# Performance work log

Measured on AMD Instinct MI355X. Metric: run time of the kernel, lower is better.

The kernel has to match this reference:

```python
import jax, jax.numpy as jnp
import numpy as np

P = 1024   # number of partitions / local models (n_terms)
K = 9      # local neighborhood size (in_dim of each LocalDNN)
W = 10     # LocalDNN width
B = 16384  # batch
F = 1024   # input feature dim (lattice sites)


def setup_inputs() -> dict:
    key = jax.random.key(0)
    ks = jax.random.split(key, 9)
    x = jax.random.normal(ks[0], (B, F), dtype=jnp.float32)
    idx = jax.random.randint(ks[1], (P, K), 0, F)  # parameter_map: per-partition feature indices
    # stacked LocalDNN parameters (one tiny MLP per partition)
    s1 = 1.0 / np.sqrt(K)
    s2 = 1.0 / np.sqrt(W)
    W1 = jax.random.uniform(ks[2], (P, K, W), jnp.float32, -s1, s1)
    b1 = jax.random.uniform(ks[3], (P, W), jnp.float32, -s1, s1)
    W2 = jax.random.uniform(ks[4], (P, W, W), jnp.float32, -s2, s2)
    b2 = jax.random.uniform(ks[5], (P, W), jnp.float32, -s2, s2)
    W3 = jax.random.uniform(ks[6], (P, W), jnp.float32, -s2, s2)   # Linear(width,1) weight
    b3 = jax.random.uniform(ks[7], (P,), jnp.float32, -s2, s2)
    sP = 1.0 / np.sqrt(P)
    w_last = jax.random.uniform(ks[8], (P,), jnp.float32, -sP, sP)  # Linear(n_terms,1,bias=False)
    return {"x": x, "idx": idx, "W1": W1, "b1": b1, "W2": W2, "b2": b2,
            "W3": W3, "b3": b3, "w_last": w_last}


def reference(x, idx, W1, b1, W2, b2, W3, b3, w_last):
    # local_map: gather per-partition features -> [B, P, K]
    xg = x[:, idx]
    # LocalDNN (depth=2): Linear(K,W) -> tanh -> Linear(W,W) -> (dropout eval no-op) -> Linear(W,1)
    h = jnp.tanh(jnp.einsum('bpk,pkw->bpw', xg, W1) + b1)      # [B,P,W]
    h = jnp.einsum('bpw,pwv->bpv', h, W2) + b2                  # [B,P,W]
    local_out = jnp.einsum('bpw,pw->bp', h, W3) + b3            # concat of per-model outputs [B,P]
    y = local_out @ w_last                                      # last_layer, flatten -> [B]
    return jnp.stack((y, jnp.full_like(y, jnp.sum(jnp.abs(w_last)))))
```

## Files before the change

kernel.cpp:

```cpp
#include <hip/hip_runtime.h>
#include <cstdint>
#include <cstddef>

#define B_TOT   16384
#define F_DIM   1024
#define P_TOT   1024
#define K_IN    9
#define W_H     10
#define TB      128
#define THREADS 1024
#define NWAVE   16
#define PGRP    2
#define PPB     (P_TOT / PGRP)
#define LSTR    1028
#define XS_BYTES (TB * LSTR)

#define REC_DW   64
#define TANH_C   2.8853900817779268f
#define F8_MAX   448.0f

typedef float f32x2 __attribute__((ext_vector_type(2)));

__device__ __forceinline__ float fast_exp2(float x) {
#if __has_builtin(__builtin_amdgcn_exp2f)
    return __builtin_amdgcn_exp2f(x);
#else
    return exp2f(x);
#endif
}
__device__ __forceinline__ float fast_rcp(float x) {
#if __has_builtin(__builtin_amdgcn_rcpf)
    return __builtin_amdgcn_rcpf(x);
#else
    return 1.0f / x;
#endif
}
__device__ __forceinline__ float sigm_r(float z) {
    return fast_rcp(fast_exp2(z) + 1.0f);
}
__device__ __forceinline__ f32x2 pkfma(f32x2 a, f32x2 b, f32x2 c) {
#if __has_builtin(__builtin_elementwise_fma)
    return __builtin_elementwise_fma(a, b, c);
#else
    return f32x2{fmaf(a[0], b[0], c[0]), fmaf(a[1], b[1], c[1])};
#endif
}
__device__ __forceinline__ f32x2 unpk8_w0(uint32_t u) {
#if __has_builtin(__builtin_amdgcn_cvt_pk_f32_fp8)
    auto v = __builtin_amdgcn_cvt_pk_f32_fp8((int)u, false);
    return f32x2{v[0], v[1]};
#else
    return f32x2{__builtin_amdgcn_cvt_f32_fp8((int)u, 0),
                 __builtin_amdgcn_cvt_f32_fp8((int)u, 1)};
#endif
}
__device__ __forceinline__ f32x2 unpk8_w1(uint32_t u) {
#if __has_builtin(__builtin_amdgcn_cvt_pk_f32_fp8)
    auto v = __builtin_amdgcn_cvt_pk_f32_fp8((int)u, true);
    return f32x2{v[0], v[1]};
#else
    return f32x2{__builtin_amdgcn_cvt_f32_fp8((int)u, 2),
                 __builtin_amdgcn_cvt_f32_fp8((int)u, 3)};
#endif
}
__device__ __forceinline__ f32x2 unpk8s(uint32_t u, int word) {
    return word ? unpk8_w1(u) : unpk8_w0(u);
}
__device__ __forceinline__ uint32_t pk2(float a0, float a1, float b0, float b1) {
    uint32_t u = (uint32_t)__builtin_amdgcn_cvt_pk_fp8_f32(a0, a1, 0, false);
    u = (uint32_t)__builtin_amdgcn_cvt_pk_fp8_f32(b0, b1, (int)u, true);
    return u;
}

__device__ __forceinline__ uint32_t rec_dword(
    int p, int dw, const int* idx,
    const float* w1, const float* b1, const float* w2, const float* b2,
    const float* w3, const float* b3, const float* wl,
    float s1, float q1)
{
    if (dw < 9)  return (uint32_t)idx[p * 9 + dw];
    if (dw == 9) return __float_as_uint(s1 * TANH_C);
    if (dw < 20) return __float_as_uint(b1[p * 10 + (dw - 10)] * TANH_C);
    if (dw == 20) {
        float bb = b3[p];
        for (int v = 0; v < 10; ++v) bb = fmaf(b2[p * 10 + v], w3[v], bb);
        float s = 0.f;
        for (int w = 0; w < 10; ++w)
            for (int v = 0; v < 10; ++v)
                s = fmaf(w2[w * 10 + v], w3[v], s);
        return __float_as_uint(wl[p] * (s + bb));
    }
    if (dw < 31) {
        const int w = dw - 21;
        float s = 0.f;
        for (int v = 0; v < 10; ++v) s = fmaf(w2[w * 10 + v], w3[v], s);
        return __float_as_uint(-2.0f * wl[p] * s);
    }
    if (dw < 32) return 0;
    if (dw < 55) {
        const int d = dw - 32, t0 = 2 * d, t1 = t0 + 1;
        const int e0 = (t0 / 5) * 10 + 2 * (t0 % 5);
        const float a0 = w1[e0] * q1, a1 = w1[e0 + 1] * q1;
        float bq0 = 0.f, bq1 = 0.f;
        if (t1 < 45) {
            const int e1 = (t1 / 5) * 10 + 2 * (t1 % 5);
            bq0 = w1[e1] * q1; bq1 = w1[e1 + 1] * q1;
        }
        return pk2(a0, a1, bq0, bq1);
    }
    return 0;
}

__global__ __launch_bounds__(64)
void prep_quant(const int* __restrict__ idx,
                const float* __restrict__ W1, const float* __restrict__ b1,
                const float* __restrict__ W2, const float* __restrict__ b2,
                const float* __restrict__ W3, const float* __restrict__ b3,
                const float* __restrict__ wl, uint32_t* __restrict__ ws)
{
    const int p = blockIdx.x;
    const int l = threadIdx.x;
    const float* w1 = W1 + p * 90;
    const float* w2 = W2 + p * 100;
    const float* w3 = W3 + p * 10;

    float m1 = (l < 90) ? fabsf(w1[l]) : 0.0f;
    if (l + 64 < 90) m1 = fmaxf(m1, fabsf(w1[l + 64]));
    #pragma unroll
    for (int off = 32; off > 0; off >>= 1)
        m1 = fmaxf(m1, __shfl_xor(m1, off));
    m1 = fmaxf(m1, 1e-20f);
    const float s1 = m1 / F8_MAX, q1 = F8_MAX / m1;

    ws[(size_t)p * REC_DW + l] =
        rec_dword(p, l, idx, w1, b1, w2, b2, w3, b3, wl, s1, q1);
}

__global__ __launch_bounds__(THREADS, 4)
void dnn_q8(const float* __restrict__ x, const uint32_t* __restrict__ ws,
            const float* __restrict__ wl, float* __restrict__ out)
{
    extern __shared__ unsigned char xs[];
    __shared__ float partial[NWAVE][TB];

    const int tid = threadIdx.x;
    const int b0  = blockIdx.x * TB;
    const int p0  = blockIdx.y * PPB;

    #pragma unroll
    for (int i = 0; i < (TB * (F_DIM / 4)) / THREADS; ++i) {
        const int q   = i * THREADS + tid;
        const int row = q >> 8;
        const int c4  = q & 255;
        const float4 v = *reinterpret_cast<const float4*>(
            x + (size_t)(b0 + row) * F_DIM + (c4 << 2));
        int pk = __builtin_amdgcn_cvt_pk_fp8_f32(v.x, v.y, 0, false);
        pk     = __builtin_amdgcn_cvt_pk_fp8_f32(v.z, v.w, pk, true);
        *reinterpret_cast<uint32_t*>(xs + row * LSTR + (c4 << 2)) = (uint32_t)pk;
    }
    __syncthreads();

    const int lane = tid & 63;
    const int wave = tid >> 6;
    const unsigned char* __restrict__ row0 = xs + lane * LSTR;
    const unsigned char* __restrict__ row1 = xs + (lane + 64) * LSTR;
    uint32_t* slots = reinterpret_cast<uint32_t*>(xs + XS_BYTES) + wave * (2 * REC_DW);

    float y0 = 0.0f, y1 = 0.0f;

    {
        const uint32_t v = ws[(size_t)(p0 + wave) * REC_DW + lane];
        slots[lane] = v;
    }
    int cur = 0;

    for (int jp = 0; jp < PPB / NWAVE; ++jp) {
        const int p = p0 + jp * NWAVE + wave;
        const uint32_t* __restrict__ rec = slots + cur * REC_DW;
        const float*    __restrict__ rf  = reinterpret_cast<const float*>(rec);

        const uint32_t stg = ws[(size_t)(p + NWAVE) * REC_DW + lane];

        float xg0[K_IN], xg1[K_IN];
        #pragma unroll
        for (int k = 0; k < K_IN; ++k) {
            const int c = (int)rec[k];
            xg0[k] = __builtin_amdgcn_cvt_f32_fp8((int)row0[c], 0);
            xg1[k] = __builtin_amdgcn_cvt_f32_fp8((int)row1[c], 0);
        }

        f32x2 H0[5], H1[5];
        #pragma unroll
        for (int j = 0; j < 5; ++j) { H0[j] = f32x2{0.f, 0.f}; H1[j] = f32x2{0.f, 0.f}; }
        #pragma unroll
        for (int k = 0; k < K_IN; ++k) {
            const f32x2 xa = {xg0[k], xg0[k]};
            const f32x2 xb = {xg1[k], xg1[k]};
            #pragma unroll
            for (int j = 0; j < 5; ++j) {
                const int t = k * 5 + j;
                const f32x2 w = unpk8s(rec[32 + (t >> 1)], t & 1);
                H0[j] = pkfma(xa, w, H0[j]);
                H1[j] = pkfma(xb, w, H1[j]);
            }
        }
        const float s1c = rf[9];
        const f32x2 s1p = {s1c, s1c};
        f32x2 r0[5], r1[5];
        #pragma unroll
        for (int j = 0; j < 5; ++j) {
            const f32x2 bj = {rf[10 + 2 * j], rf[11 + 2 * j]};
            const f32x2 z0 = pkfma(H0[j], s1p, bj);
            const f32x2 z1 = pkfma(H1[j], s1p, bj);
            r0[j] = f32x2{sigm_r(z0[0]), sigm_r(z0[1])};
            r1[j] = f32x2{sigm_r(z1[0]), sigm_r(z1[1])};
        }

        const float c0 = rf[20];
        f32x2 A0 = {0.f, 0.f}, A1 = {0.f, 0.f};
        #pragma unroll
        for (int j = 0; j < 5; ++j) {
            const f32x2 cwj = {rf[21 + 2 * j], rf[22 + 2 * j]};
            A0 = pkfma(cwj, r0[j], A0);
            A1 = pkfma(cwj, r1[j], A1);
        }
        y0 += c0 + A0[0] + A0[1];
        y1 += c0 + A1[0] + A1[1];

        slots[(cur ^ 1) * REC_DW + lane] = stg;
        cur ^= 1;
    }

    partial[wave][lane]      = y0;
    partial[wave][lane + 64] = y1;
    __syncthreads();

    if (tid < TB) {
        float s = 0.0f;
        #pragma unroll
        for (int w = 0; w < NWAVE; ++w) s += partial[w][tid];
        atomicAdd(&out[b0 + tid], s);
    }

    if (blockIdx.y == 0 && tid < 64) {
        float sa = 0.0f;
        #pragma unroll
        for (int i = 0; i < P_TOT / 64; ++i) sa += fabsf(wl[tid + 64 * i]);
        #pragma unroll
        for (int off = 32; off > 0; off >>= 1) sa += __shfl_down(sa, off);
        sa = __shfl(sa, 0);
        out[B_TOT + b0 + tid]      = sa;
        out[B_TOT + b0 + 64 + tid] = sa;
    }
}

extern "C" void kernel_launch(void* const* d_in, const int* in_sizes, int n_in,
                              void* d_out, int out_size, void* d_ws, size_t ws_size,
                              hipStream_t stream)
{
    const float* x  = (const float*)d_in[0];
    const int*   idx= (const int*)  d_in[1];
    const float* W1 = (const float*)d_in[2];
    const float* b1 = (const float*)d_in[3];
    const float* W2 = (const float*)d_in[4];
    const float* b2 = (const float*)d_in[5];
    const float* W3 = (const float*)d_in[6];
    const float* b3 = (const float*)d_in[7];
    const float* wl = (const float*)d_in[8];
    float* out = (float*)d_out;
    uint32_t* ws = (uint32_t*)d_ws;

    (void)hipMemsetAsync(out, 0, B_TOT * sizeof(float), stream);

    prep_quant<<<P_TOT, 64, 0, stream>>>(idx, W1, b1, W2, b2, W3, b3, wl, ws);

    const int smem = XS_BYTES + NWAVE * 2 * REC_DW * 4;
    (void)hipFuncSetAttribute(reinterpret_cast<const void*>(dnn_q8),
                              hipFuncAttributeMaxDynamicSharedMemorySize, smem);

    dim3 grid(B_TOT / TB, PGRP);
    dnn_q8<<<grid, THREADS, smem, stream>>>(x, ws, wl, out);
}
```

Baseline: 105.0 us.

## Halve batch tile to one row per lane and raise occupancy bound

Shrinks the per-block batch tile from 128 to 64 rows, so each lane processes a single batch row instead of two. The launch bound goes from 4 to 8 blocks per CU to exploit the smaller LDS footprint and lower register use. The cost is that each weight record loaded into LDS is now reused across half as many rows, and the grid has twice as many blocks doing atomics. The |w_last| sum is folded into the tid<TB branch.

Result: slower. 119.2 us (+13.6%).

```diff
diff --git a/kernel.cpp b/kernel.cpp
--- a/kernel.cpp
+++ b/kernel.cpp
@@ -7,7 +7,7 @@
 #define P_TOT   1024
 #define K_IN    9
 #define W_H     10
-#define TB      128
+#define TB      64
 #define THREADS 1024
 #define NWAVE   16
 #define PGRP    2
@@ -136,7 +136,7 @@
         rec_dword(p, l, idx, w1, b1, w2, b2, w3, b3, wl, s1, q1);
 }
 
-__global__ __launch_bounds__(THREADS, 4)
+__global__ __launch_bounds__(THREADS, 8)
 void dnn_q8(const float* __restrict__ x, const uint32_t* __restrict__ ws,
             const float* __restrict__ wl, float* __restrict__ out)
 {
@@ -162,16 +162,12 @@
 
     const int lane = tid & 63;
     const int wave = tid >> 6;
-    const unsigned char* __restrict__ row0 = xs + lane * LSTR;
-    const unsigned char* __restrict__ row1 = xs + (lane + 64) * LSTR;
+    const unsigned char* __restrict__ myrow = xs + lane * LSTR;
     uint32_t* slots = reinterpret_cast<uint32_t*>(xs + XS_BYTES) + wave * (2 * REC_DW);
 
-    float y0 = 0.0f, y1 = 0.0f;
-
-    {
-        const uint32_t v = ws[(size_t)(p0 + wave) * REC_DW + lane];
-        slots[lane] = v;
-    }
+    float yacc = 0.0f;
+
+    slots[lane] = ws[(size_t)(p0 + wave) * REC_DW + lane];
     int cur = 0;
 
     for (int jp = 0; jp < PPB / NWAVE; ++jp) {
@@ -181,58 +177,47 @@
 
         const uint32_t stg = ws[(size_t)(p + NWAVE) * REC_DW + lane];
 
-        float xg0[K_IN], xg1[K_IN];
+        float xg[K_IN];
+        #pragma unroll
+        for (int k = 0; k < K_IN; ++k)
+            xg[k] = __builtin_amdgcn_cvt_f32_fp8((int)myrow[(int)rec[k]], 0);
+
+        f32x2 H[5];
+        #pragma unroll
+        for (int j = 0; j < 5; ++j) H[j] = f32x2{0.f, 0.f};
         #pragma unroll
         for (int k = 0; k < K_IN; ++k) {
-            const int c = (int)rec[k];
-            xg0[k] = __builtin_amdgcn_cvt_f32_fp8((int)row0[c], 0);
-            xg1[k] = __builtin_amdgcn_cvt_f32_fp8((int)row1[c], 0);
-        }
-
-        f32x2 H0[5], H1[5];
-        #pragma unroll
-        for (int j = 0; j < 5; ++j) { H0[j] = f32x2{0.f, 0.f}; H1[j] = f32x2{0.f, 0.f}; }
-        #pragma unroll
-        for (int k = 0; k < K_IN; ++k) {
-            const f32x2 xa = {xg0[k], xg0[k]};
-            const f32x2 xb = {xg1[k], xg1[k]};
+            const f32x2 xk = {xg[k], xg[k]};
             #pragma unroll
             for (int j = 0; j < 5; ++j) {
                 const int t = k * 5 + j;
-                const f32x2 w = unpk8s(rec[32 + (t >> 1)], t & 1);
-                H0[j] = pkfma(xa, w, H0[j]);
-                H1[j] = pkfma(xb, w, H1[j]);
+                H[j] = pkfma(xk, unpk8s(rec[32 + (t >> 1)], t & 1), H[j]);
             }
         }
         const float s1c = rf[9];
         const f32x2 s1p = {s1c, s1c};
-        f32x2 r0[5], r1[5];
+        f32x2 r[5];
         #pragma unroll
         for (int j = 0; j < 5; ++j) {
             const f32x2 bj = {rf[10 + 2 * j], rf[11 + 2 * j]};
-            const f32x2 z0 = pkfma(H0[j], s1p, bj);
-            const f32x2 z1 = pkfma(H1[j], s1p, bj);
-            r0[j] = f32x2{sigm_r(z0[0]), sigm_r(z0[1])};
-            r1[j] = f32x2{sigm_r(z1[0]), sigm_r(z1[1])};
+            const f32x2 z = pkfma(H[j], s1p, bj);
+            r[j] = f32x2{sigm_r(z[0]), sigm_r(z[1])};
         }
 
         const float c0 = rf[20];
-        f32x2 A0 = {0.f, 0.f}, A1 = {0.f, 0.f};
+        f32x2 A = {0.f, 0.f};
         #pragma unroll
         for (int j = 0; j < 5; ++j) {
             const f32x2 cwj = {rf[21 + 2 * j], rf[22 + 2 * j]};
-            A0 = pkfma(cwj, r0[j], A0);
-            A1 = pkfma(cwj, r1[j], A1);
-        }
-        y0 += c0 + A0[0] + A0[1];
-        y1 += c0 + A1[0] + A1[1];
+            A = pkfma(cwj, r[j], A);
+        }
+        yacc += c0 + A[0] + A[1];
 
         slots[(cur ^ 1) * REC_DW + lane] = stg;
         cur ^= 1;
     }
 
-    partial[wave][lane]      = y0;
-    partial[wave][lane + 64] = y1;
+    partial[wave][lane] = yacc;
     __syncthreads();
 
     if (tid < TB) {
@@ -240,17 +225,16 @@
         #pragma unroll
         for (int w = 0; w < NWAVE; ++w) s += partial[w][tid];
         atomicAdd(&out[b0 + tid], s);
-    }
-
-    if (blockIdx.y == 0 && tid < 64) {
-        float sa = 0.0f;
-        #pragma unroll
-        for (int i = 0; i < P_TOT / 64; ++i) sa += fabsf(wl[tid + 64 * i]);
-        #pragma unroll
-        for (int off = 32; off > 0; off >>= 1) sa += __shfl_down(sa, off);
-        sa = __shfl(sa, 0);
-        out[B_TOT + b0 + tid]      = sa;
-        out[B_TOT + b0 + 64 + tid] = sa;
+
+        if (blockIdx.y == 0) {
+            float sa = 0.0f;
+            #pragma unroll
+            for (int i = 0; i < P_TOT / TB; ++i) sa += fabsf(wl[tid + TB * i]);
+            #pragma unroll
+            for (int off = 32; off > 0; off >>= 1) sa += __shfl_down(sa, off);
+            sa = __shfl(sa, 0);
+            out[B_TOT + b0 + tid] = sa;
+        }
     }
 }
 
```
